# Kernel tuning notes

Measured on AMD Instinct MI355X. Metric: run time of the kernel, lower is better.

Reference implementation:

```python
import jax, jax.numpy as jnp
import numpy as np

B, S, DIM, H, C = 1, 1024, 4096, 32, 8
HD = DIM // H  # 128
NEG = -1e9


def setup_inputs() -> dict:
    key = jax.random.key(0)
    ks = jax.random.split(key, 8)
    scale = 0.02
    x = jax.random.normal(ks[0], (B, S, DIM), jnp.float32)
    wq = jax.random.normal(ks[1], (DIM, DIM), jnp.float32) * scale
    wk = jax.random.normal(ks[2], (DIM, DIM), jnp.float32) * scale
    wv = jax.random.normal(ks[3], (DIM, DIM), jnp.float32) * scale
    wo = jax.random.normal(ks[4], (DIM, DIM), jnp.float32) * scale
    # RoPE tables (theta=10000), matching precompute_freqs_cis
    inv = 1.0 / (10000.0 ** (np.arange(0, HD, 2, dtype=np.float32) / HD))  # [HD/2]
    ang = np.arange(S, dtype=np.float32)[:, None] * inv[None, :]  # [S, HD/2]
    freqs_cos = jnp.asarray(np.cos(ang))
    freqs_sin = jnp.asarray(np.sin(ang))
    # causal mask used at prefill (start_pos == 0)
    mask = jnp.where(jnp.triu(jnp.ones((S, S), bool), k=1), jnp.float32(NEG), 0.0)
    # cluster labels: ensure every cluster non-empty; rep = first head with label
    rng = np.random.default_rng(0)
    lab = np.concatenate([np.arange(C), rng.integers(0, C, H - C)]).astype(np.int32)
    rep = np.array([np.where(lab == c)[0][0] for c in range(C)], dtype=np.int32)
    return {
        "x": x, "wq": wq, "wk": wk, "wv": wv, "wo": wo,
        "freqs_cos": freqs_cos, "freqs_sin": freqs_sin, "mask": mask,
        "cluster_assignment": jnp.asarray(lab), "rep_heads": jnp.asarray(rep),
        "start_pos": 0,
    }


def _rope(x, cos, sin):
    # x: [b, s, h, d]; cos/sin: [s, d/2]; interleaved complex multiply
    xr, xi = x[..., ::2], x[..., 1::2]
    cos = cos[None, :, None, :]
    sin = sin[None, :, None, :]
    orr = xr * cos - xi * sin
    oi = xr * sin + xi * cos
    return jnp.stack([orr, oi], axis=-1).reshape(x.shape)


def reference(x, wq, wk, wv, wo, freqs_cos, freqs_sin, mask,
              cluster_assignment, rep_heads, start_pos):
    b, s, dim = x.shape
    h, d = H, HD
    xq = (x @ wq.T).reshape(b, s, h, d)
    xk = (x @ wk.T).reshape(b, s, h, d)
    xv = (x @ wv.T).reshape(b, s, h, d)
    xq = _rope(xq, freqs_cos, freqs_sin)
    xk = _rope(xk, freqs_cos, freqs_sin)
    xqh = jnp.transpose(xq, (0, 2, 1, 3))  # [b, h, s, d]
    xkh = jnp.transpose(xk, (0, 2, 1, 3))
    vh = jnp.transpose(xv, (0, 2, 1, 3))
    # CHAI: gather representative head per cluster, score once per cluster
    xq_new = xqh[:, rep_heads]  # [b, C, s, d]
    xk_new = xkh[:, rep_heads]
    sc = jnp.einsum("bcqd,bckd->bcqk", xq_new, xk_new) / jnp.sqrt(jnp.float32(d))
    # scatter cluster scores back to every member head (pure gather by label)
    scores = sc[:, cluster_assignment]  # [b, h, s, s]
    scores = scores + mask[None, None]
    p = jax.nn.softmax(scores.astype(jnp.float32), axis=-1).astype(x.dtype)
    out = jnp.einsum("bhqk,bhkd->bhqd", p, vh)
    out = jnp.transpose(out, (0, 2, 1, 3)).reshape(b, s, h * d)
    return out @ wo.T
```

## Files before the change

### kernel.cpp

```cpp
#include <hip/hip_runtime.h>

typedef __bf16 bf16x8 __attribute__((ext_vector_type(8)));
typedef float f32x4 __attribute__((ext_vector_type(4)));

#define BM 128
#define BN 128
#define BK 64

__device__ __forceinline__ unsigned short f2bf(float f) {
    union { float f; unsigned int u; } x; x.f = f;
    unsigned int u = x.u;
    u += 0x7fffu + ((u >> 16) & 1u);
    return (unsigned short)(u >> 16);
}

__device__ __forceinline__ float bf2f(unsigned short h) {
    union { unsigned int u; float f; } x; x.u = ((unsigned int)h) << 16;
    return x.f;
}

__device__ __forceinline__ void async_copy16(const void* g, void* l) {
    __builtin_amdgcn_global_load_lds(
        (const __attribute__((address_space(1))) void*)(uintptr_t)g,
        (__attribute__((address_space(3))) void*)(uintptr_t)l, 16, 0, 0);
}


__global__ void cvt_bf16(const float* __restrict__ s, unsigned short* __restrict__ d, long n4) {
    long i = (long)blockIdx.x * blockDim.x + threadIdx.x;
    if (i >= n4) return;
    float4 v = ((const float4*)s)[i];
    ushort4 o;
    o.x = f2bf(v.x); o.y = f2bf(v.y); o.z = f2bf(v.z); o.w = f2bf(v.w);
    ((ushort4*)d)[i] = o;
}

__global__ void build_wqkv(const float* __restrict__ wq, const float* __restrict__ wk,
                           const float* __restrict__ wv, const int* __restrict__ rep,
                           unsigned short* __restrict__ dst) {
    long i = (long)blockIdx.x * blockDim.x + threadIdx.x;
    int r = (int)(i >> 10), c4 = (int)(i & 1023);
    const float* src;
    if (r < 1024)      src = wq + ((long)(rep[r >> 7] * 128 + (r & 127)) << 12);
    else if (r < 2048) src = wk + ((long)(rep[(r - 1024) >> 7] * 128 + (r & 127)) << 12);
    else               src = wv + ((long)(r - 2048) << 12);
    float4 v = ((const float4*)src)[c4];
    ushort4 o;
    o.x = f2bf(v.x); o.y = f2bf(v.y); o.z = f2bf(v.z); o.w = f2bf(v.w);
    ((ushort4*)(dst + ((long)r << 12)))[c4] = o;
}


template<bool F32OUT, int MODE>
__global__ __launch_bounds__(256, 2) void gemm_bt(
    const unsigned short* __restrict__ A, const unsigned short* __restrict__ B,
    void* __restrict__ Cv, int K, int lda, int ldb, int ldc,
    long long aZ, long long bZ, long long cZ, const int* __restrict__ aIdx,
    int kOffZ, int nby) {
    __shared__ unsigned short As[BM * BK];
    __shared__ unsigned short Bs[BN * BK];

    int L = blockIdx.x;
    int q8 = gridDim.x >> 3;
    int wk_ = (L & 7) * q8 + (L >> 3);
    int bmi = wk_ & 7;
    int t2 = wk_ >> 3;
    int bni = t2 % nby;
    int z = t2 / nby;

    if (MODE == 1 && bni > bmi) return;

    A += (aIdx ? (long long)aIdx[z] : (long long)z) * aZ;
    B += (long long)z * bZ;
    int bm = bmi * BM;
    int bn = bni * BN;
    int t = threadIdx.x;
    int lane = t & 63;
    int w = t >> 6;
    int wr = (w >> 1) * 64, wc = (w & 1) * 64;

    int kt0 = z * kOffZ;
    int kEnd = kt0 + K;
    if (MODE == 2) kEnd = kt0 + min(K, bm + BM);

    f32x4 acc[4][4] = {};

    for (int kt = kt0; kt < kEnd; kt += BK) {
#pragma unroll
        for (int i = 0; i < 4; ++i) {
            int f = i * 256 + t;
            int row = f >> 3;
            int c8 = f & 7;
            async_copy16(A + (long)(bm + row) * lda + kt + c8 * 8, &As[f * 8]);
            async_copy16(B + (long)(bn + row) * ldb + kt + c8 * 8, &Bs[f * 8]);
        }
        asm volatile("s_waitcnt vmcnt(0)" ::: "memory");
        __syncthreads();
#pragma unroll
        for (int kk = 0; kk < BK; kk += 32) {
            bf16x8 a[4], b[4];
            int r0 = lane & 15;
            int kof = kk + ((lane >> 4) << 3);
#pragma unroll
            for (int m = 0; m < 4; ++m)
                a[m] = *(const bf16x8*)&As[(wr + m * 16 + r0) * BK + kof];
#pragma unroll
            for (int n = 0; n < 4; ++n)
                b[n] = *(const bf16x8*)&Bs[(wc + n * 16 + r0) * BK + kof];
#pragma unroll
            for (int m = 0; m < 4; ++m)
#pragma unroll
                for (int n = 0; n < 4; ++n)
                    acc[m][n] = __builtin_amdgcn_mfma_f32_16x16x32_bf16(a[m], b[n], acc[m][n], 0, 0, 0);
        }
        __syncthreads();
    }

    int cl = lane & 15;
    int rbase = (lane >> 4) << 2;
    if (F32OUT) {
        float* C = (float*)Cv + (long long)z * cZ;
#pragma unroll
        for (int m = 0; m < 4; ++m)
#pragma unroll
            for (int n = 0; n < 4; ++n)
#pragma unroll
                for (int j = 0; j < 4; ++j)
                    C[(long)(bm + wr + m * 16 + rbase + j) * ldc + (bn + wc + n * 16 + cl)] = acc[m][n][j];
    } else {
        unsigned short* C = (unsigned short*)Cv + (long long)z * cZ;
#pragma unroll
        for (int m = 0; m < 4; ++m)
#pragma unroll
            for (int n = 0; n < 4; ++n)
#pragma unroll
                for (int j = 0; j < 4; ++j)
                    C[(long)(bm + wr + m * 16 + rbase + j) * ldc + (bn + wc + n * 16 + cl)] = f2bf(acc[m][n][j]);
    }
}

__global__ void reduce_rope(unsigned short* __restrict__ qkv,
                            const unsigned short* __restrict__ part1,
                            const float* __restrict__ fc, const float* __restrict__ fs,
                            int haveSplit) {
    int s = blockIdx.y;
    int cc = (blockIdx.x * 256 + threadIdx.x) * 8;
    long base = (long)s * 6144 + cc;
    ushort4 a0 = *(const ushort4*)(qkv + base);
    ushort4 a1 = *(const ushort4*)(qkv + base + 4);
    float f[8] = { bf2f(a0.x), bf2f(a0.y), bf2f(a0.z), bf2f(a0.w),
                   bf2f(a1.x), bf2f(a1.y), bf2f(a1.z), bf2f(a1.w) };
    if (haveSplit) {
        ushort4 b0 = *(const ushort4*)(part1 + base);
        ushort4 b1 = *(const ushort4*)(part1 + base + 4);
        f[0] += bf2f(b0.x); f[1] += bf2f(b0.y); f[2] += bf2f(b0.z); f[3] += bf2f(b0.w);
        f[4] += bf2f(b1.x); f[5] += bf2f(b1.y); f[6] += bf2f(b1.z); f[7] += bf2f(b1.w);
    }
    if (cc < 2048) {
        int i0 = (cc & 127) >> 1;
        const float* cp = fc + (s << 6) + i0;
        const float* sp = fs + (s << 6) + i0;
#pragma unroll
        for (int p = 0; p < 4; ++p) {
            float co = cp[p], sn = sp[p];
            float x0 = f[2 * p], x1 = f[2 * p + 1];
            f[2 * p] = x0 * co - x1 * sn;
            f[2 * p + 1] = x0 * sn + x1 * co;
        }
    }
    ushort4 o0 = { f2bf(f[0]), f2bf(f[1]), f2bf(f[2]), f2bf(f[3]) };
    ushort4 o1 = { f2bf(f[4]), f2bf(f[5]), f2bf(f[6]), f2bf(f[7]) };
    *(ushort4*)(qkv + base) = o0;
    *(ushort4*)(qkv + base + 4) = o1;
}

__global__ void reduce_out(const float* __restrict__ p, float* __restrict__ out, int n4) {
    int i = blockIdx.x * 256 + threadIdx.x;
    if (i >= n4) return;
    float4 a = ((const float4*)p)[i];
    float4 b = ((const float4*)(p + (long)4194304))[i];
    float4 o = { a.x + b.x, a.y + b.y, a.z + b.z, a.w + b.w };
    ((float4*)out)[i] = o;
}

__global__ void transpose_v(const unsigned short* __restrict__ qkv, unsigned short* __restrict__ vt) {
    __shared__ unsigned short tile[32][33];
    int h = blockIdx.z, d0 = blockIdx.x * 32, s0 = blockIdx.y * 32;
    int tx = threadIdx.x & 31, ty = threadIdx.x >> 5;
#pragma unroll
    for (int i = 0; i < 32; i += 8)
        tile[ty + i][tx] = qkv[(long)(s0 + ty + i) * 6144 + 2048 + h * 128 + d0 + tx];
    __syncthreads();
#pragma unroll
    for (int i = 0; i < 32; i += 8)
        vt[(long)h * 131072 + (long)(d0 + ty + i) * 1024 + s0 + tx] = tile[tx][ty + i];
}

__global__ __launch_bounds__(256) void softmax_causal(const float* __restrict__ sc,
                                                      unsigned short* __restrict__ P) {
    int i = blockIdx.x;
    int c = blockIdx.y;
    long base = ((long)c << 20) + ((long)i << 10);
    const float* row = sc + base;
    unsigned short* prow = P + base;
    int t = threadIdx.x;
    const float alpha = 0.08838834764831845f;
    int nj = i >> 8;

    float v[4];
    float mx = -3.4e38f;
    for (int j0 = 0; j0 <= nj; ++j0) {
        int j = j0 * 256 + t;
        float x = row[j] * alpha;
        v[j0] = (j <= i) ? x : -3.4e38f;
        mx = fmaxf(mx, v[j0]);
    }
#pragma unroll
    for (int o = 32; o > 0; o >>= 1) mx = fmaxf(mx, __shfl_xor(mx, o));
    __shared__ float red[4];
    int w = t >> 6, lane = t & 63;
    if (lane == 0) red[w] = mx;
    __syncthreads();
    mx = fmaxf(fmaxf(red[0], red[1]), fmaxf(red[2], red[3]));

    float e[4];
    float sum = 0.f;
    for (int j0 = 0; j0 <= nj; ++j0) {
        e[j0] = (v[j0] > -1e37f) ? __expf(v[j0] - mx) : 0.f;
        sum += e[j0];
    }
#pragma unroll
    for (int o = 32; o > 0; o >>= 1) sum += __shfl_xor(sum, o);
    __syncthreads();
    if (lane == 0) red[w] = sum;
    __syncthreads();
    sum = red[0] + red[1] + red[2] + red[3];
    float inv = 1.f / sum;
    for (int j0 = 0; j0 <= nj; ++j0) {
        int j = j0 * 256 + t;
        prow[j] = f2bf(e[j0] * inv);
    }
}


extern "C" void kernel_launch(void* const* d_in, const int* in_sizes, int n_in,
                              void* d_out, int out_size, void* d_ws, size_t ws_size,
                              hipStream_t stream) {
    const float* x  = (const float*)d_in[0];
    const float* wq = (const float*)d_in[1];
    const float* wk = (const float*)d_in[2];
    const float* wv = (const float*)d_in[3];
    const float* wo = (const float*)d_in[4];
    const float* fc = (const float*)d_in[5];
    const float* fs = (const float*)d_in[6];
    const int* lab = (const int*)d_in[8];
    const int* rep = (const int*)d_in[9];
    float* out = (float*)d_out;

    char* ws = (char*)d_ws;
    unsigned short* xb    = (unsigned short*)(ws);
    unsigned short* wqkvb = (unsigned short*)(ws + 8388608);
    unsigned short* wob   = (unsigned short*)(ws + 58720256);
    unsigned short* qkv_s = (unsigned short*)(ws + 92274688);
    unsigned short* part1 = (unsigned short*)(ws + 104857600);
    unsigned short* vt    = part1;
    float* scores         = (float*)(ws + 8388608);
    unsigned short* P     = (unsigned short*)(ws + 41943040);
    float* opart          = (float*)(ws + 8388608);
    unsigned short* attn  = xb;

    bool splitK = ws_size >= (size_t)117440512;

    cvt_bf16<<<4096, 256, 0, stream>>>(x, xb, (long)1024 * 4096 / 4);
    build_wqkv<<<24576, 256, 0, stream>>>(wq, wk, wv, rep, wqkvb);
    cvt_bf16<<<16384, 256, 0, stream>>>(wo, wob, (long)4096 * 4096 / 4);

    if (splitK) {
        gemm_bt<false, 0><<<768, 256, 0, stream>>>(
            xb, wqkvb, qkv_s, 2048, 4096, 4096, 6144, 0, 0, 6291456, nullptr, 2048, 48);
    } else {
        gemm_bt<false, 0><<<384, 256, 0, stream>>>(
            xb, wqkvb, qkv_s, 4096, 4096, 4096, 6144, 0, 0, 0, nullptr, 0, 48);
    }

    reduce_rope<<<dim3(3, 1024), 256, 0, stream>>>(qkv_s, part1, fc, fs, splitK ? 1 : 0);
    transpose_v<<<dim3(4, 32, 32), 256, 0, stream>>>(qkv_s, vt);

    gemm_bt<true, 1><<<512, 256, 0, stream>>>(
        qkv_s, qkv_s + 1024, scores, 128, 6144, 6144, 1024,
        128, 128, 1048576, nullptr, 0, 8);

    softmax_causal<<<dim3(1024, 8), 256, 0, stream>>>(scores, P);

    gemm_bt<false, 2><<<256, 256, 0, stream>>>(
        P, vt, attn, 1024, 1024, 1024, 4096,
        1048576, 131072, 128, lab, 0, 1);

    if (splitK) {
        gemm_bt<true, 0><<<512, 256, 0, stream>>>(
            attn, wob, opart, 2048, 4096, 4096, 4096, 0, 0, 4194304, nullptr, 2048, 32);
        reduce_out<<<4096, 256, 0, stream>>>(opart, out, 1048576);
    } else {
        gemm_bt<true, 0><<<256, 256, 0, stream>>>(
            attn, wob, out, 4096, 4096, 4096, 4096, 0, 0, 0, nullptr, 0, 32);
    }
}
```

Before: 233.4 us.

## Fuse conversion kernels, raise split-K to 4 with bf16 partials

Merges the three fp32-to-bf16 conversion launches into one kernel. Raises split-K for the QKV and output projections from 2 to 4 to put more blocks on the GPU, and generalises the rope reduction to sum any number of partials. Output-projection partials are now stored in bf16 instead of fp32, which cuts reduction traffic but rounds each partial sum to bf16 before the fp32 final add. The output path also always uses split-K 4 regardless of workspace size, so it relies on the workspace being large enough.

```diff
diff --git a/kernel.cpp b/kernel.cpp
--- a/kernel.cpp
+++ b/kernel.cpp
@@ -25,29 +25,36 @@
         (__attribute__((address_space(3))) void*)(uintptr_t)l, 16, 0, 0);
 }
 
-
-__global__ void cvt_bf16(const float* __restrict__ s, unsigned short* __restrict__ d, long n4) {
-    long i = (long)blockIdx.x * blockDim.x + threadIdx.x;
-    if (i >= n4) return;
-    float4 v = ((const float4*)s)[i];
-    ushort4 o;
-    o.x = f2bf(v.x); o.y = f2bf(v.y); o.z = f2bf(v.z); o.w = f2bf(v.w);
-    ((ushort4*)d)[i] = o;
-}
-
-__global__ void build_wqkv(const float* __restrict__ wq, const float* __restrict__ wk,
-                           const float* __restrict__ wv, const int* __restrict__ rep,
-                           unsigned short* __restrict__ dst) {
-    long i = (long)blockIdx.x * blockDim.x + threadIdx.x;
-    int r = (int)(i >> 10), c4 = (int)(i & 1023);
+__global__ void cvt_all(const float* __restrict__ x, const float* __restrict__ wq,
+                        const float* __restrict__ wk, const float* __restrict__ wv,
+                        const float* __restrict__ wo, const int* __restrict__ rep,
+                        unsigned short* __restrict__ xb, unsigned short* __restrict__ wqkvb,
+                        unsigned short* __restrict__ wob) {
+    long i = (long)blockIdx.x * 256 + threadIdx.x;
     const float* src;
-    if (r < 1024)      src = wq + ((long)(rep[r >> 7] * 128 + (r & 127)) << 12);
-    else if (r < 2048) src = wk + ((long)(rep[(r - 1024) >> 7] * 128 + (r & 127)) << 12);
-    else               src = wv + ((long)(r - 2048) << 12);
-    float4 v = ((const float4*)src)[c4];
-    ushort4 o;
-    o.x = f2bf(v.x); o.y = f2bf(v.y); o.z = f2bf(v.z); o.w = f2bf(v.w);
-    ((ushort4*)(dst + ((long)r << 12)))[c4] = o;
+    unsigned short* dst;
+    long j;
+    if (i < 1048576) {
+        j = i;
+        src = x; dst = xb;
+    } else if (i < 7340032) {
+        j = i - 1048576;
+        int r = (int)(j >> 10), c4 = (int)(j & 1023);
+        const float* s;
+        if (r < 1024)      s = wq + ((long)(rep[r >> 7] * 128 + (r & 127)) << 12);
+        else if (r < 2048) s = wk + ((long)(rep[(r - 1024) >> 7] * 128 + (r & 127)) << 12);
+        else               s = wv + ((long)(r - 2048) << 12);
+        float4 v = ((const float4*)s)[c4];
+        ushort4 o = { f2bf(v.x), f2bf(v.y), f2bf(v.z), f2bf(v.w) };
+        ((ushort4*)(wqkvb + ((long)r << 12)))[c4] = o;
+        return;
+    } else {
+        j = i - 7340032;
+        src = wo; dst = wob;
+    }
+    float4 v = ((const float4*)src)[j];
+    ushort4 o = { f2bf(v.x), f2bf(v.y), f2bf(v.z), f2bf(v.w) };
+    ((ushort4*)dst)[j] = o;
 }
 
 
@@ -140,9 +147,8 @@
 }
 
 __global__ void reduce_rope(unsigned short* __restrict__ qkv,
-                            const unsigned short* __restrict__ part1,
                             const float* __restrict__ fc, const float* __restrict__ fs,
-                            int haveSplit) {
+                            int nsplit) {
     int s = blockIdx.y;
     int cc = (blockIdx.x * 256 + threadIdx.x) * 8;
     long base = (long)s * 6144 + cc;
@@ -150,9 +156,10 @@
     ushort4 a1 = *(const ushort4*)(qkv + base + 4);
     float f[8] = { bf2f(a0.x), bf2f(a0.y), bf2f(a0.z), bf2f(a0.w),
                    bf2f(a1.x), bf2f(a1.y), bf2f(a1.z), bf2f(a1.w) };
-    if (haveSplit) {
-        ushort4 b0 = *(const ushort4*)(part1 + base);
-        ushort4 b1 = *(const ushort4*)(part1 + base + 4);
+    for (int z = 1; z < nsplit; ++z) {
+        const unsigned short* p = qkv + (long)z * 6291456;
+        ushort4 b0 = *(const ushort4*)(p + base);
+        ushort4 b1 = *(const ushort4*)(p + base + 4);
         f[0] += bf2f(b0.x); f[1] += bf2f(b0.y); f[2] += bf2f(b0.z); f[3] += bf2f(b0.w);
         f[4] += bf2f(b1.x); f[5] += bf2f(b1.y); f[6] += bf2f(b1.z); f[7] += bf2f(b1.w);
     }
@@ -174,12 +181,17 @@
     *(ushort4*)(qkv + base + 4) = o1;
 }
 
-__global__ void reduce_out(const float* __restrict__ p, float* __restrict__ out, int n4) {
-    int i = blockIdx.x * 256 + threadIdx.x;
-    if (i >= n4) return;
-    float4 a = ((const float4*)p)[i];
-    float4 b = ((const float4*)(p + (long)4194304))[i];
-    float4 o = { a.x + b.x, a.y + b.y, a.z + b.z, a.w + b.w };
+__global__ void reduce_out4(const unsigned short* __restrict__ p, float* __restrict__ out) {
+    long i = (long)blockIdx.x * 256 + threadIdx.x;
+    ushort4 a = ((const ushort4*)p)[i];
+    ushort4 b = ((const ushort4*)(p + 4194304))[i];
+    ushort4 c = ((const ushort4*)(p + 8388608))[i];
+    ushort4 d = ((const ushort4*)(p + 12582912))[i];
+    float4 o;
+    o.x = bf2f(a.x) + bf2f(b.x) + bf2f(c.x) + bf2f(d.x);
+    o.y = bf2f(a.y) + bf2f(b.y) + bf2f(c.y) + bf2f(d.y);
+    o.z = bf2f(a.z) + bf2f(b.z) + bf2f(c.z) + bf2f(d.z);
+    o.w = bf2f(a.w) + bf2f(b.w) + bf2f(c.w) + bf2f(d.w);
     ((float4*)out)[i] = o;
 }
 
@@ -262,20 +274,21 @@
     unsigned short* wqkvb = (unsigned short*)(ws + 8388608);
     unsigned short* wob   = (unsigned short*)(ws + 58720256);
     unsigned short* qkv_s = (unsigned short*)(ws + 92274688);
-    unsigned short* part1 = (unsigned short*)(ws + 104857600);
-    unsigned short* vt    = part1;
+    unsigned short* vt    = (unsigned short*)(ws + 104857600);
     float* scores         = (float*)(ws + 8388608);
     unsigned short* P     = (unsigned short*)(ws + 41943040);
-    float* opart          = (float*)(ws + 8388608);
+    unsigned short* opart = (unsigned short*)(ws + 8388608);
     unsigned short* attn  = xb;
 
-    bool splitK = ws_size >= (size_t)117440512;
-
-    cvt_bf16<<<4096, 256, 0, stream>>>(x, xb, (long)1024 * 4096 / 4);
-    build_wqkv<<<24576, 256, 0, stream>>>(wq, wk, wv, rep, wqkvb);
-    cvt_bf16<<<16384, 256, 0, stream>>>(wo, wob, (long)4096 * 4096 / 4);
-
-    if (splitK) {
+    int skQ = (ws_size >= (size_t)142606336) ? 4
+            : (ws_size >= (size_t)117440512) ? 2 : 1;
+
+    cvt_all<<<45056, 256, 0, stream>>>(x, wq, wk, wv, wo, rep, xb, wqkvb, wob);
+
+    if (skQ == 4) {
+        gemm_bt<false, 0><<<1536, 256, 0, stream>>>(
+            xb, wqkvb, qkv_s, 1024, 4096, 4096, 6144, 0, 0, 6291456, nullptr, 1024, 48);
+    } else if (skQ == 2) {
         gemm_bt<false, 0><<<768, 256, 0, stream>>>(
             xb, wqkvb, qkv_s, 2048, 4096, 4096, 6144, 0, 0, 6291456, nullptr, 2048, 48);
     } else {
@@ -283,7 +296,7 @@
             xb, wqkvb, qkv_s, 4096, 4096, 4096, 6144, 0, 0, 0, nullptr, 0, 48);
     }
 
-    reduce_rope<<<dim3(3, 1024), 256, 0, stream>>>(qkv_s, part1, fc, fs, splitK ? 1 : 0);
+    reduce_rope<<<dim3(3, 1024), 256, 0, stream>>>(qkv_s, fc, fs, skQ);
     transpose_v<<<dim3(4, 32, 32), 256, 0, stream>>>(qkv_s, vt);
 
     gemm_bt<true, 1><<<512, 256, 0, stream>>>(
@@ -296,12 +309,7 @@
         P, vt, attn, 1024, 1024, 1024, 4096,
         1048576, 131072, 128, lab, 0, 1);
 
-    if (splitK) {
-        gemm_bt<true, 0><<<512, 256, 0, stream>>>(
-            attn, wob, opart, 2048, 4096, 4096, 4096, 0, 0, 4194304, nullptr, 2048, 32);
-        reduce_out<<<4096, 256, 0, stream>>>(opart, out, 1048576);
-    } else {
-        gemm_bt<true, 0><<<256, 256, 0, stream>>>(
-            attn, wob, out, 4096, 4096, 4096, 4096, 0, 0, 0, nullptr, 0, 32);
-    }
-}
+    gemm_bt<false, 0><<<1024, 256, 0, stream>>>(
+        attn, wob, opart, 1024, 4096, 4096, 4096, 0, 0, 4194304, nullptr, 1024, 32);
+    reduce_out4<<<4096, 256, 0, stream>>>(opart, out);
+}
```

After: 225.5 us. 1.03x faster.
